# Kernel optimization log

Hardware: AMD Instinct MI355X
Metric: run time of the kernel (lower is better)

## Reference

```python
import jax, jax.numpy as jnp
import numpy as np

N_TOKENS = 65536
HIDDEN = 1024
N_EXPERTS = 64
EPS = 1e-12  # matches F.normalize default eps
NEG_BIG = float(jnp.finfo(jnp.bfloat16).max)  # -torch.finfo(bfloat16).max sentinel


def setup_inputs() -> dict:
    key = jax.random.key(0)
    k1, k2 = jax.random.split(key)
    x = jax.random.normal(k1, (N_TOKENS, HIDDEN), dtype=jnp.float32)
    sim_matrix = jax.random.normal(k2, (HIDDEN, N_EXPERTS), dtype=jnp.float32)  # nn.Parameter(randn)
    gates = jnp.zeros((N_EXPERTS,), dtype=jnp.float32)  # nn.Parameter(zeros)
    return {"x": x, "sim_matrix": sim_matrix, "gates": gates}


def _l2norm(v, axis):
    n = jnp.sqrt(jnp.sum(v * v, axis=axis, keepdims=True))
    return v / jnp.maximum(n, EPS)


def reference(x, sim_matrix, gates):
    # cosine-similarity logits: [N, E]
    logits = jnp.matmul(_l2norm(x, -1), _l2norm(sim_matrix, 0))
    thr = jax.nn.sigmoid(gates)                      # [E]
    pre_activation_logits = logits - thr             # [N, E]
    gated = jax.nn.relu(pre_activation_logits)
    # STE: forward hard 0/1, backward identity
    hard = (gated > 0).astype(x.dtype)
    activation_mask = gated + jax.lax.stop_gradient(hard - gated)
    # topk fallback for rows with zero active experts (vectorized scatter)
    inactive = jnp.sum(hard, axis=1) == 0            # [N]
    k_fallback = N_EXPERTS // 2
    _, topk_idx = jax.lax.top_k(logits, k_fallback)  # [N, k]
    rows = jnp.arange(x.shape[0])
    fb = jnp.zeros_like(logits).at[rows[:, None], topk_idx].set(1.0)
    activation_mask = jnp.where(inactive[:, None], fb, activation_mask)
    # masked softmax over active experts
    masked = jnp.where(activation_mask > 0, gated, -NEG_BIG)
    active_expert_probs = jax.nn.softmax(masked, axis=-1)
    return active_expert_probs, pre_activation_logits, activation_mask
```

## Files before the change

kernel.cpp:

```cpp
#include <hip/hip_runtime.h>
#include <math.h>

#define N_TOK   65536
#define HID     1024
#define NEXP    64
#define EPSF    1e-12f
#define EPSW    4e-5f

typedef __attribute__((ext_vector_type(8))) short s16x8;
typedef __attribute__((ext_vector_type(4))) float f32x4;

__device__ __forceinline__ unsigned short f2bf(float f) {
    unsigned u = __float_as_uint(f);
    unsigned r = u + 0x7fffu + ((u >> 16) & 1u);
    return (unsigned short)(r >> 16);
}
__device__ __forceinline__ float bf2f(unsigned short h) {
    return __uint_as_float(((unsigned)h) << 16);
}
__device__ __forceinline__ unsigned enc_key(float f) {
    unsigned u = __float_as_uint(f);
    return (u & 0x80000000u) ? ~u : (u | 0x80000000u);
}
__device__ __forceinline__ float dec_key(unsigned k) {
    unsigned u = (k & 0x80000000u) ? (k ^ 0x80000000u) : ~k;
    return __uint_as_float(u);
}

__global__ __launch_bounds__(256) void prep_kernel(const float* __restrict__ sim,
                                                   const float* __restrict__ gates,
                                                   float* __restrict__ ws) {
    __shared__ float partial[4][64];
    int e = threadIdx.x & 63;
    int q = threadIdx.x >> 6;
    float s = 0.f;
    for (int h = q * 256; h < q * 256 + 256; ++h) {
        float v = sim[h * NEXP + e];
        s += v * v;
    }
    partial[q][e] = s;
    __syncthreads();
    if (threadIdx.x < 64) {
        float ss = partial[0][e] + partial[1][e] + partial[2][e] + partial[3][e];
        ws[e] = 1.0f / fmaxf(sqrtf(ss), EPSF);
        ws[64 + e] = 1.0f / (1.0f + expf(-gates[e]));
    }
}

__global__ __launch_bounds__(256) void prep2n_kernel(const float* __restrict__ sim,
                                                     const float* __restrict__ ws_ro,
                                                     float* __restrict__ wn) {
    int idx = blockIdx.x * 256 + threadIdx.x;
    wn[idx] = sim[idx] * ws_ro[idx & 63];
}

__global__ __launch_bounds__(256) void prep3_kernel(const float* __restrict__ wn,
                                                    unsigned short* __restrict__ wbh,
                                                    unsigned short* __restrict__ wbl) {
    int i = blockIdx.x * 256 + threadIdx.x;
    int j    = i & 7;
    int lane = (i >> 3) & 63;
    int nt   = (i >> 9) & 3;
    int kt   = i >> 11;
    int k = kt * 32 + ((lane >> 4) & 3) * 8 + j;
    int e = nt * 16 + (lane & 15);
    float v = wn[k * NEXP + e];
    unsigned short h = f2bf(v);
    unsigned short l = f2bf(v - bf2f(h));
    wbh[i] = h; wbl[i] = l;
}

__global__ __launch_bounds__(256) void gate_v12_kernel(const float* __restrict__ x,
                                                       const float* __restrict__ wn,
                                                       const unsigned short* __restrict__ wbh,
                                                       const unsigned short* __restrict__ wbl,
                                                       const float* __restrict__ prep,
                                                       float* __restrict__ out) {
    __shared__ __align__(16) float lg[64][68];
    __shared__ __align__(16) float xrow[HID];
    __shared__ float ss_l[64];
    __shared__ float thr_l[64];
    __shared__ int   flags_i[64];
    __shared__ float part[256];

    const int tid   = threadIdx.x;
    const int lane  = tid & 63;
    const int wv    = tid >> 6;
    const int tbase = blockIdx.x * 64;

    const int arow = lane & 15;
    const int aoct = lane >> 4;
    const float* xg = x + (size_t)(tbase + wv * 16 + arow) * HID + aoct * 8;

    if (tid < 64) thr_l[tid] = prep[64 + tid];

    f32x4 acc[4];
#pragma unroll
    for (int nt = 0; nt < 4; ++nt) acc[nt] = (f32x4){0.f, 0.f, 0.f, 0.f};
    float ss = 0.f;

    const s16x8* bh_g = (const s16x8*)wbh;
    const s16x8* bl_g = (const s16x8*)wbl;

    float4 xv0 = *(const float4*)(xg);
    float4 xv1 = *(const float4*)(xg + 4);

#pragma unroll 2
    for (int c = 0; c < 32; ++c) {
        float4 nx0, nx1;
        if (c < 31) {
            nx0 = *(const float4*)(xg + (c + 1) * 32);
            nx1 = *(const float4*)(xg + (c + 1) * 32 + 4);
        }
        s16x8 bh[4], bl[4];
#pragma unroll
        for (int nt = 0; nt < 4; ++nt) {
            bh[nt] = bh_g[(c * 4 + nt) * 64 + lane];
            bl[nt] = bl_g[(c * 4 + nt) * 64 + lane];
        }
        const float a[8] = { xv0.x, xv0.y, xv0.z, xv0.w, xv1.x, xv1.y, xv1.z, xv1.w };
        s16x8 ah, al;
#pragma unroll
        for (int i = 0; i < 8; ++i) {
            ss = fmaf(a[i], a[i], ss);
            unsigned short h = f2bf(a[i]);
            ah[i] = (short)h;
            al[i] = (short)f2bf(a[i] - bf2f(h));
        }
#pragma unroll
        for (int nt = 0; nt < 4; ++nt)
            acc[nt] = __builtin_amdgcn_mfma_f32_16x16x32_bf16(al, bh[nt], acc[nt], 0, 0, 0);
#pragma unroll
        for (int nt = 0; nt < 4; ++nt)
            acc[nt] = __builtin_amdgcn_mfma_f32_16x16x32_bf16(ah, bl[nt], acc[nt], 0, 0, 0);
#pragma unroll
        for (int nt = 0; nt < 4; ++nt)
            acc[nt] = __builtin_amdgcn_mfma_f32_16x16x32_bf16(ah, bh[nt], acc[nt], 0, 0, 0);
        xv0 = nx0; xv1 = nx1;
    }

    ss += __shfl_xor(ss, 16);
    ss += __shfl_xor(ss, 32);
    if (lane < 16) ss_l[wv * 16 + lane] = ss;

#pragma unroll
    for (int nt = 0; nt < 4; ++nt)
#pragma unroll
        for (int r = 0; r < 4; ++r)
            lg[wv * 16 + aoct * 4 + r][nt * 16 + arow] = acc[nt][r];
    __syncthreads();

    const int tg = lane >> 3;
    const int eg = lane & 7;
    const int e0 = eg * 8;
    const size_t out_pre  = (size_t)N_TOK * NEXP;
    const size_t out_mask = 2 * (size_t)N_TOK * NEXP;

#pragma unroll
    for (int j = 0; j < 2; ++j) {
        const int tl = wv * 16 + tg * 2 + j;
        const int t  = tbase + tl;
        const float inv = 1.0f / fmaxf(sqrtf(ss_l[tl]), EPSF);

        float logit[8], pre[8];
        int active[8];
        int myact = 0;
#pragma unroll
        for (int i = 0; i < 8; ++i) {
            logit[i] = lg[tl][e0 + i] * inv;
            pre[i]   = logit[i] - thr_l[e0 + i];
            active[i] = pre[i] > 0.f;
            myact += active[i];
        }
        *(float4*)&out[out_pre + (size_t)t * NEXP + e0]     = make_float4(pre[0], pre[1], pre[2], pre[3]);
        *(float4*)&out[out_pre + (size_t)t * NEXP + e0 + 4] = make_float4(pre[4], pre[5], pre[6], pre[7]);

        int rowact = myact;
        rowact += __shfl_xor(rowact, 1, 8);
        rowact += __shfl_xor(rowact, 2, 8);
        rowact += __shfl_xor(rowact, 4, 8);

        int flag;
        if (rowact > 0) {
            float mn = 1e30f;
#pragma unroll
            for (int i = 0; i < 8; ++i) mn = fminf(mn, fabsf(pre[i]));
            mn = fminf(mn, __shfl_xor(mn, 1, 8));
            mn = fminf(mn, __shfl_xor(mn, 2, 8));
            mn = fminf(mn, __shfl_xor(mn, 4, 8));
            flag = (mn <= EPSW);
            if (!flag) {
                float gated[8], probs[8], mask[8];
#pragma unroll
                for (int i = 0; i < 8; ++i) gated[i] = fmaxf(pre[i], 0.f);
                float m = -INFINITY;
#pragma unroll
                for (int i = 0; i < 8; ++i) m = fmaxf(m, active[i] ? gated[i] : -INFINITY);
                m = fmaxf(m, __shfl_xor(m, 1, 8));
                m = fmaxf(m, __shfl_xor(m, 2, 8));
                m = fmaxf(m, __shfl_xor(m, 4, 8));
                float s = 0.f;
#pragma unroll
                for (int i = 0; i < 8; ++i) {
                    float ev = active[i] ? expf(gated[i] - m) : 0.f;
                    probs[i] = ev; s += ev;
                }
                s += __shfl_xor(s, 1, 8);
                s += __shfl_xor(s, 2, 8);
                s += __shfl_xor(s, 4, 8);
                float rs = 1.0f / s;
#pragma unroll
                for (int i = 0; i < 8; ++i) { probs[i] *= rs; mask[i] = active[i] ? 1.f : 0.f; }
                size_t row = (size_t)t * NEXP + e0;
                *(float4*)&out[row]                = make_float4(probs[0], probs[1], probs[2], probs[3]);
                *(float4*)&out[row + 4]            = make_float4(probs[4], probs[5], probs[6], probs[7]);
                *(float4*)&out[out_mask + row]     = make_float4(mask[0], mask[1], mask[2], mask[3]);
                *(float4*)&out[out_mask + row + 4] = make_float4(mask[4], mask[5], mask[6], mask[7]);
            }
        } else {
            unsigned key[8];
#pragma unroll
            for (int i = 0; i < 8; ++i) key[i] = enc_key(logit[i]);
            unsigned cand = 0u;
            for (int bit = 31; bit >= 0; --bit) {
                unsigned test = cand | (1u << bit);
                int c = 0;
#pragma unroll
                for (int i = 0; i < 8; ++i) c += (key[i] >= test);
                c += __shfl_xor(c, 1, 8);
                c += __shfl_xor(c, 2, 8);
                c += __shfl_xor(c, 4, 8);
                if (c >= 32) cand = test;
            }
            const float val32 = dec_key(cand);
            int nhi = 0, nlo = 0, nam = 0;
#pragma unroll
            for (int i = 0; i < 8; ++i) {
                nhi += logit[i] > val32 + EPSW;
                nlo += logit[i] > val32 - EPSW;
                nam += pre[i] > -EPSW;
            }
            nhi += __shfl_xor(nhi, 1, 8); nhi += __shfl_xor(nhi, 2, 8); nhi += __shfl_xor(nhi, 4, 8);
            nlo += __shfl_xor(nlo, 1, 8); nlo += __shfl_xor(nlo, 2, 8); nlo += __shfl_xor(nlo, 4, 8);
            nam += __shfl_xor(nam, 1, 8); nam += __shfl_xor(nam, 2, 8); nam += __shfl_xor(nam, 4, 8);
            flag = !(nhi == 31 && nlo == 32) || (nam > 0);
            if (!flag) {
                float probs[8], mask[8];
#pragma unroll
                for (int i = 0; i < 8; ++i) {
                    int sel = logit[i] > val32 - EPSW;
                    mask[i]  = sel ? 1.f : 0.f;
                    probs[i] = sel ? 0.03125f : 0.f;
                }
                size_t row = (size_t)t * NEXP + e0;
                *(float4*)&out[row]                = make_float4(probs[0], probs[1], probs[2], probs[3]);
                *(float4*)&out[row + 4]            = make_float4(probs[4], probs[5], probs[6], probs[7]);
                *(float4*)&out[out_mask + row]     = make_float4(mask[0], mask[1], mask[2], mask[3]);
                *(float4*)&out[out_mask + row + 4] = make_float4(mask[4], mask[5], mask[6], mask[7]);
            }
        }
        if (eg == 0) flags_i[tl] = flag;
    }
    __syncthreads();

    for (int tf = 0; tf < 64; ++tf) {
        if (flags_i[tf] == 0) continue;
        {
            float4 v = *(const float4*)&x[(size_t)(tbase + tf) * HID + tid * 4];
            *(float4*)&xrow[tid * 4] = v;
        }
        __syncthreads();
        const int e = tid & 63;
        const int q = tid >> 6;
        const float* wp = wn + (size_t)q * 256 * NEXP + e;
        const float* xr = xrow + q * 256;
        float dot = 0.f;
#pragma unroll 8
        for (int k2 = 0; k2 < 256; ++k2)
            dot = fmaf(xr[k2], wp[(size_t)k2 * NEXP], dot);
        part[q * 64 + e] = dot;
        __syncthreads();
        if (tid < 64) {
            const float inv = 1.0f / fmaxf(sqrtf(ss_l[tf]), EPSF);
            const float lgv = ((part[e] + part[64 + e]) + (part[128 + e] + part[192 + e])) * inv;
            const float pr = lgv - thr_l[e];
            unsigned long long act = __ballot(pr > 0.f);
            float probs, mask;
            if (act) {
                float g = fmaxf(pr, 0.f);
                float mv = (pr > 0.f) ? g : -INFINITY;
#pragma unroll
                for (int d = 1; d < 64; d <<= 1) mv = fmaxf(mv, __shfl_xor(mv, d));
                float ex = (pr > 0.f) ? expf(g - mv) : 0.f;
                float s = ex;
#pragma unroll
                for (int d = 1; d < 64; d <<= 1) s += __shfl_xor(s, d);
                probs = ex / s;
                mask  = (pr > 0.f) ? 1.f : 0.f;
            } else {
                unsigned key = enc_key(lgv);
                unsigned cand = 0u;
                for (int bit = 31; bit >= 0; --bit) {
                    unsigned test = cand | (1u << bit);
                    int c = __popcll(__ballot(key >= test));
                    if (c >= 32) cand = test;
                }
                int need = 32 - __popcll(__ballot(key > cand));
                unsigned long long em = __ballot(key == cand);
                unsigned long long mlt = e ? (~0ull >> (64 - e)) : 0ull;
                int below = __popcll(em & mlt);
                int sel = (key > cand) || ((key == cand) && (below < need));
                probs = sel ? 0.03125f : 0.f;
                mask  = sel ? 1.f : 0.f;
            }
            size_t row = (size_t)(tbase + tf) * NEXP;
            out[row + e] = probs;
            out[out_mask + row + e] = mask;
        }
        __syncthreads();
    }
}

__global__ __launch_bounds__(256) void gate_v10_kernel(const float* __restrict__ x,
                                                       const float* __restrict__ wn,
                                                       const float* __restrict__ prep,
                                                       float* __restrict__ out) {
    __shared__ __align__(16) float smem[8704];
    float* ss_part = smem + 8448;
    const int tid  = threadIdx.x;
    const int lane = tid & 63;
    const int wv   = tid >> 6;
    const int tg   = lane >> 3;
    const int eg   = lane & 7;
    const int e0   = eg * 8;
    const int tbase = blockIdx.x * 64;
    const int kbase = wv * 256;
    float* xsw = smem + wv * 2112;
    const float4* xq4 = (const float4*)(x + (size_t)(tbase + lane) * HID + kbase);
    float acc[8][8];
#pragma unroll
    for (int t = 0; t < 8; ++t)
#pragma unroll
        for (int e = 0; e < 8; ++e) acc[t][e] = 0.f;
    float ss = 0.f;
    {
        float4 f0 = xq4[0], f1 = xq4[1];
        const float4* wq4 = (const float4*)(wn + (size_t)kbase * NEXP) + lane * 2;
        float4 w0 = wq4[0], w1 = wq4[1];
        const float a[8] = { f0.x, f0.y, f0.z, f0.w, f1.x, f1.y, f1.z, f1.w };
#pragma unroll
        for (int i = 0; i < 8; ++i) { ss = fmaf(a[i], a[i], ss); xsw[i * 68 + lane] = a[i]; }
        *(float4*)&xsw[1088 + lane * 8]     = w0;
        *(float4*)&xsw[1088 + lane * 8 + 4] = w1;
    }
#define FMA8x8(XA, XB, WA, WB)                                              \
    do {                                                                    \
        const float xv_[8] = { XA.x, XA.y, XA.z, XA.w, XB.x, XB.y, XB.z, XB.w }; \
        const float wv_[8] = { WA.x, WA.y, WA.z, WA.w, WB.x, WB.y, WB.z, WB.w }; \
        _Pragma("unroll")                                                   \
        for (int t_ = 0; t_ < 8; ++t_)                                      \
            _Pragma("unroll")                                               \
            for (int e_ = 0; e_ < 8; ++e_)                                  \
                acc[t_][e_] = fmaf(xv_[t_], wv_[e_], acc[t_][e_]);          \
    } while (0)
#pragma unroll 1
    for (int c = 0; c < 32; ++c) {
        float4 sx0, sx1, sw0, sw1;
        if (c < 31) {
            sx0 = xq4[(c + 1) * 2];
            sx1 = xq4[(c + 1) * 2 + 1];
            const float4* wq4 = (const float4*)(wn + (size_t)(kbase + (c + 1) * 8) * NEXP) + lane * 2;
            sw0 = wq4[0]; sw1 = wq4[1];
        }
        const float* xb = xsw + (c & 1) * 544;
        const float* wb = xsw + 1088 + (c & 1) * 512;
#pragma unroll
        for (int k = 0; k < 8; ++k) {
            const float4 xa = *(const float4*)&xb[k * 68 + tg * 8];
            const float4 xc = *(const float4*)&xb[k * 68 + tg * 8 + 4];
            const float4 wa = *(const float4*)&wb[k * 64 + e0];
            const float4 wc = *(const float4*)&wb[k * 64 + e0 + 4];
            FMA8x8(xa, xc, wa, wc);
        }
        if (c < 31) {
            float* xn = xsw + ((c + 1) & 1) * 544;
            float* wl = xsw + 1088 + ((c + 1) & 1) * 512;
            const float a[8] = { sx0.x, sx0.y, sx0.z, sx0.w, sx1.x, sx1.y, sx1.z, sx1.w };
#pragma unroll
            for (int i = 0; i < 8; ++i) { ss = fmaf(a[i], a[i], ss); xn[i * 68 + lane] = a[i]; }
            *(float4*)&wl[lane * 8]     = sw0;
            *(float4*)&wl[lane * 8 + 4] = sw1;
        }
    }
#undef FMA8x8
    ss_part[wv * 64 + lane] = ss;
    __syncthreads();
    if (wv < 2) {
        float* reg = smem + wv * 4224;
#pragma unroll
        for (int j = 0; j < 8; ++j) {
            float* p = &reg[(tg * 8 + j) * 65 + e0];
            *(float4*)(p)     = make_float4(acc[j][0], acc[j][1], acc[j][2], acc[j][3]);
            *(float4*)(p + 4) = make_float4(acc[j][4], acc[j][5], acc[j][6], acc[j][7]);
        }
    }
    __syncthreads();
    if (wv >= 2) {
        float* reg = smem + (wv - 2) * 4224;
#pragma unroll
        for (int j = 0; j < 8; ++j) {
            float* p = &reg[(tg * 8 + j) * 65 + e0];
            float4 p0 = *(const float4*)(p);
            float4 p1 = *(const float4*)(p + 4);
            p0.x += acc[j][0]; p0.y += acc[j][1]; p0.z += acc[j][2]; p0.w += acc[j][3];
            p1.x += acc[j][4]; p1.y += acc[j][5]; p1.z += acc[j][6]; p1.w += acc[j][7];
            *(float4*)(p) = p0; *(float4*)(p + 4) = p1;
        }
    }
    __syncthreads();
    float thr[8];
#pragma unroll
    for (int i = 0; i < 8; ++i) thr[i] = prep[64 + e0 + i];
    const size_t out_pre  = (size_t)N_TOK * NEXP;
    const size_t out_mask = 2 * (size_t)N_TOK * NEXP;
    const float* regA = smem;
    const float* regB = smem + 4224;
#pragma unroll
    for (int j = 0; j < 2; ++j) {
        const int tl = wv * 16 + tg * 2 + j;
        const int t  = tbase + tl;
        const float sst = (ss_part[tl] + ss_part[64 + tl]) + (ss_part[128 + tl] + ss_part[192 + tl]);
        const float inv = 1.0f / fmaxf(sqrtf(sst), EPSF);
        float4 aA0 = *(const float4*)&regA[tl * 65 + e0];
        float4 aA1 = *(const float4*)&regA[tl * 65 + e0 + 4];
        float4 aB0 = *(const float4*)&regB[tl * 65 + e0];
        float4 aB1 = *(const float4*)&regB[tl * 65 + e0 + 4];
        float logit[8] = { (aA0.x + aB0.x) * inv, (aA0.y + aB0.y) * inv,
                           (aA0.z + aB0.z) * inv, (aA0.w + aB0.w) * inv,
                           (aA1.x + aB1.x) * inv, (aA1.y + aB1.y) * inv,
                           (aA1.z + aB1.z) * inv, (aA1.w + aB1.w) * inv };
        float pre[8], gated[8];
        int active[8];
        int myact = 0;
#pragma unroll
        for (int i = 0; i < 8; ++i) {
            pre[i]   = logit[i] - thr[i];
            gated[i] = fmaxf(pre[i], 0.f);
            active[i] = pre[i] > 0.f;
            myact += active[i];
        }
        int rowact = myact;
        rowact += __shfl_xor(rowact, 1, 8);
        rowact += __shfl_xor(rowact, 2, 8);
        rowact += __shfl_xor(rowact, 4, 8);
        float probs[8], mask[8];
        if (rowact > 0) {
            float m = -INFINITY;
#pragma unroll
            for (int i = 0; i < 8; ++i) m = fmaxf(m, active[i] ? gated[i] : -INFINITY);
            m = fmaxf(m, __shfl_xor(m, 1, 8));
            m = fmaxf(m, __shfl_xor(m, 2, 8));
            m = fmaxf(m, __shfl_xor(m, 4, 8));
            float s = 0.f;
#pragma unroll
            for (int i = 0; i < 8; ++i) { float ev = active[i] ? expf(gated[i] - m) : 0.f; probs[i] = ev; s += ev; }
            s += __shfl_xor(s, 1, 8);
            s += __shfl_xor(s, 2, 8);
            s += __shfl_xor(s, 4, 8);
            float rs = 1.0f / s;
#pragma unroll
            for (int i = 0; i < 8; ++i) { probs[i] *= rs; mask[i] = active[i] ? 1.f : 0.f; }
        } else {
            unsigned key[8];
#pragma unroll
            for (int i = 0; i < 8; ++i) key[i] = enc_key(logit[i]);
            unsigned cand = 0u;
            for (int bit = 31; bit >= 0; --bit) {
                unsigned test = cand | (1u << bit);
                int c = 0;
#pragma unroll
                for (int i = 0; i < 8; ++i) c += (key[i] >= test);
                c += __shfl_xor(c, 1, 8);
                c += __shfl_xor(c, 2, 8);
                c += __shfl_xor(c, 4, 8);
                if (c >= 32) cand = test;
            }
            int cgt = 0;
#pragma unroll
            for (int i = 0; i < 8; ++i) cgt += (key[i] > cand);
            cgt += __shfl_xor(cgt, 1, 8);
            cgt += __shfl_xor(cgt, 2, 8);
            cgt += __shfl_xor(cgt, 4, 8);
            int need_eq = 32 - cgt;
            int eqc = 0;
#pragma unroll
            for (int i = 0; i < 8; ++i) eqc += (key[i] == cand);
            int scan = eqc, tmp;
            tmp = __shfl_up(scan, 1, 8); if (eg >= 1) scan += tmp;
            tmp = __shfl_up(scan, 2, 8); if (eg >= 2) scan += tmp;
            tmp = __shfl_up(scan, 4, 8); if (eg >= 4) scan += tmp;
            int run = scan - eqc;
#pragma unroll
            for (int i = 0; i < 8; ++i) {
                int sel = (key[i] > cand) || ((key[i] == cand) && (run < need_eq));
                run += (key[i] == cand);
                mask[i]  = sel ? 1.f : 0.f;
                probs[i] = sel ? 0.03125f : 0.f;
            }
        }
        const size_t row = (size_t)t * NEXP + e0;
        *(float4*)&out[row]                = make_float4(probs[0], probs[1], probs[2], probs[3]);
        *(float4*)&out[row + 4]            = make_float4(probs[4], probs[5], probs[6], probs[7]);
        *(float4*)&out[out_pre + row]      = make_float4(pre[0], pre[1], pre[2], pre[3]);
        *(float4*)&out[out_pre + row + 4]  = make_float4(pre[4], pre[5], pre[6], pre[7]);
        *(float4*)&out[out_mask + row]     = make_float4(mask[0], mask[1], mask[2], mask[3]);
        *(float4*)&out[out_mask + row + 4] = make_float4(mask[4], mask[5], mask[6], mask[7]);
    }
}

extern "C" void kernel_launch(void* const* d_in, const int* in_sizes, int n_in,
                              void* d_out, int out_size, void* d_ws, size_t ws_size,
                              hipStream_t stream) {
    (void)in_sizes; (void)n_in; (void)out_size;
    const float* x     = (const float*)d_in[0];
    const float* sim   = (const float*)d_in[1];
    const float* gates = (const float*)d_in[2];
    float* out = (float*)d_out;
    float* ws  = (float*)d_ws;

    hipLaunchKernelGGL(prep_kernel, dim3(1), dim3(256), 0, stream, sim, gates, ws);

    const size_t need_v10 = 512 + (size_t)HID * NEXP * sizeof(float);
    const size_t need_v12 = need_v10 + 2 * (size_t)HID * NEXP * sizeof(short);
    if (ws_size >= need_v12) {
        float* wn = ws + 128;
        unsigned short* wbh = (unsigned short*)((char*)ws + 512 + (size_t)HID * NEXP * 4);
        unsigned short* wbl = wbh + (size_t)HID * NEXP;
        hipLaunchKernelGGL(prep2n_kernel, dim3(HID * NEXP / 256), dim3(256), 0, stream,
                           sim, ws, wn);
        hipLaunchKernelGGL(prep3_kernel, dim3(HID * NEXP / 256), dim3(256), 0, stream,
                           wn, wbh, wbl);
        hipLaunchKernelGGL(gate_v12_kernel, dim3(N_TOK / 64), dim3(256), 0, stream,
                           x, wn, wbh, wbl, ws, out);
    } else {
        float* wn = ws + 128;
        hipLaunchKernelGGL(prep2n_kernel, dim3(HID * NEXP / 256), dim3(256), 0, stream,
                           sim, ws, wn);
        hipLaunchKernelGGL(gate_v10_kernel, dim3(N_TOK / 64), dim3(256), 0, stream,
                           x, wn, ws, out);
    }
}
```

Measured before the change: 197.0 us.

## Stage x and weight tiles in double-buffered LDS, split waves by expert tile

The main GEMM loop is restructured. Each wave now owns one 16-expert slice across all 64 tokens, instead of one 16-token slice across all experts. The x rows are converted to bf16 hi/lo once per element and stored in double-buffered shared memory, along with the split weight tiles, and all waves reuse them from there. This removes the redundant global weight loads per wave and overlaps the next chunk's global loads with the current MFMAs. The cost is a __syncthreads on every K step, extra LDS traffic, and a per-row sum of squares that now needs a four-way partial reduction.

```diff
diff --git a/kernel.cpp b/kernel.cpp
--- a/kernel.cpp
+++ b/kernel.cpp
@@ -70,84 +70,129 @@
     wbh[i] = h; wbl[i] = l;
 }
 
-__global__ __launch_bounds__(256) void gate_v12_kernel(const float* __restrict__ x,
+__global__ __launch_bounds__(256) void gate_v14_kernel(const float* __restrict__ x,
                                                        const float* __restrict__ wn,
                                                        const unsigned short* __restrict__ wbh,
                                                        const unsigned short* __restrict__ wbl,
                                                        const float* __restrict__ prep,
                                                        float* __restrict__ out) {
-    __shared__ __align__(16) float lg[64][68];
-    __shared__ __align__(16) float xrow[HID];
-    __shared__ float ss_l[64];
-    __shared__ float thr_l[64];
-    __shared__ int   flags_i[64];
-    __shared__ float part[256];
+    __shared__ __align__(16) float smem[8768];
+    unsigned short* AhU = (unsigned short*)smem;
+    unsigned short* AlU = (unsigned short*)(smem + 2080);
+    unsigned short* BhU = (unsigned short*)(smem + 4352);
+    unsigned short* BlU = (unsigned short*)(smem + 6400);
+    float* xrow    = smem + 4352;
+    float* part    = smem + 5376;
+    int*   flags_i = (int*)(smem + 5632);
+    float* ss_part = smem + 8448;
+    float* thr_l   = smem + 8704;
 
     const int tid   = threadIdx.x;
     const int lane  = tid & 63;
     const int wv    = tid >> 6;
     const int tbase = blockIdx.x * 64;
 
-    const int arow = lane & 15;
-    const int aoct = lane >> 4;
-    const float* xg = x + (size_t)(tbase + wv * 16 + arow) * HID + aoct * 8;
+    const int t_st = tid & 63;
+    const int q_st = tid >> 6;
+    const int fl   = (t_st & 15) + 16 * q_st;
+    const int mt   = t_st >> 4;
+    const float* xrow_g = x + (size_t)(tbase + t_st) * HID;
 
     if (tid < 64) thr_l[tid] = prep[64 + tid];
 
     f32x4 acc[4];
 #pragma unroll
-    for (int nt = 0; nt < 4; ++nt) acc[nt] = (f32x4){0.f, 0.f, 0.f, 0.f};
+    for (int m = 0; m < 4; ++m) acc[m] = (f32x4){0.f, 0.f, 0.f, 0.f};
     float ss = 0.f;
 
     const s16x8* bh_g = (const s16x8*)wbh;
     const s16x8* bl_g = (const s16x8*)wbl;
 
-    float4 xv0 = *(const float4*)(xg);
-    float4 xv1 = *(const float4*)(xg + 4);
-
-#pragma unroll 2
-    for (int c = 0; c < 32; ++c) {
-        float4 nx0, nx1;
-        if (c < 31) {
-            nx0 = *(const float4*)(xg + (c + 1) * 32);
-            nx1 = *(const float4*)(xg + (c + 1) * 32 + 4);
-        }
-        s16x8 bh[4], bl[4];
-#pragma unroll
-        for (int nt = 0; nt < 4; ++nt) {
-            bh[nt] = bh_g[(c * 4 + nt) * 64 + lane];
-            bl[nt] = bl_g[(c * 4 + nt) * 64 + lane];
-        }
-        const float a[8] = { xv0.x, xv0.y, xv0.z, xv0.w, xv1.x, xv1.y, xv1.z, xv1.w };
-        s16x8 ah, al;
+    {
+        float4 v0 = *(const float4*)(xrow_g + q_st * 8);
+        float4 v1 = *(const float4*)(xrow_g + q_st * 8 + 4);
+        s16x8 b0h = bh_g[tid];
+        s16x8 b0l = bl_g[tid];
+        const float a[8] = { v0.x, v0.y, v0.z, v0.w, v1.x, v1.y, v1.z, v1.w };
+        s16x8 hv, lv;
 #pragma unroll
         for (int i = 0; i < 8; ++i) {
             ss = fmaf(a[i], a[i], ss);
             unsigned short h = f2bf(a[i]);
-            ah[i] = (short)h;
-            al[i] = (short)f2bf(a[i] - bf2f(h));
-        }
-#pragma unroll
-        for (int nt = 0; nt < 4; ++nt)
-            acc[nt] = __builtin_amdgcn_mfma_f32_16x16x32_bf16(al, bh[nt], acc[nt], 0, 0, 0);
-#pragma unroll
-        for (int nt = 0; nt < 4; ++nt)
-            acc[nt] = __builtin_amdgcn_mfma_f32_16x16x32_bf16(ah, bl[nt], acc[nt], 0, 0, 0);
-#pragma unroll
-        for (int nt = 0; nt < 4; ++nt)
-            acc[nt] = __builtin_amdgcn_mfma_f32_16x16x32_bf16(ah, bh[nt], acc[nt], 0, 0, 0);
-        xv0 = nx0; xv1 = nx1;
-    }
-
-    ss += __shfl_xor(ss, 16);
-    ss += __shfl_xor(ss, 32);
-    if (lane < 16) ss_l[wv * 16 + lane] = ss;
-
-#pragma unroll
-    for (int nt = 0; nt < 4; ++nt)
-#pragma unroll
-        for (int r = 0; r < 4; ++r)
-            lg[wv * 16 + aoct * 4 + r][nt * 16 + arow] = acc[nt][r];
+            hv[i] = (short)h;
+            lv[i] = (short)f2bf(a[i] - bf2f(h));
+        }
+        int slot = mt * 65 + fl;
+        *(s16x8*)&AhU[slot * 8] = hv;
+        *(s16x8*)&AlU[slot * 8] = lv;
+        *(s16x8*)&BhU[tid * 8] = b0h;
+        *(s16x8*)&BlU[tid * 8] = b0l;
+    }
+    __syncthreads();
+
+#pragma unroll 1
+    for (int c = 0; c < 32; ++c) {
+        const int buf = c & 1;
+        float4 nv0, nv1;
+        s16x8 nBh, nBl;
+        if (c < 31) {
+            nv0 = *(const float4*)(xrow_g + (c + 1) * 32 + q_st * 8);
+            nv1 = *(const float4*)(xrow_g + (c + 1) * 32 + q_st * 8 + 4);
+            nBh = bh_g[(c + 1) * 256 + tid];
+            nBl = bl_g[(c + 1) * 256 + tid];
+        }
+
+        s16x8 ah[4], al[4];
+#pragma unroll
+        for (int m = 0; m < 4; ++m) {
+            int base = ((buf << 2) + m) * 65 * 8 + lane * 8;
+            ah[m] = *(const s16x8*)&AhU[base];
+            al[m] = *(const s16x8*)&AlU[base];
+        }
+        s16x8 bhf = *(const s16x8*)&BhU[(buf * 256 + wv * 64 + lane) * 8];
+        s16x8 blf = *(const s16x8*)&BlU[(buf * 256 + wv * 64 + lane) * 8];
+#pragma unroll
+        for (int m = 0; m < 4; ++m)
+            acc[m] = __builtin_amdgcn_mfma_f32_16x16x32_bf16(al[m], bhf, acc[m], 0, 0, 0);
+#pragma unroll
+        for (int m = 0; m < 4; ++m)
+            acc[m] = __builtin_amdgcn_mfma_f32_16x16x32_bf16(ah[m], blf, acc[m], 0, 0, 0);
+#pragma unroll
+        for (int m = 0; m < 4; ++m)
+            acc[m] = __builtin_amdgcn_mfma_f32_16x16x32_bf16(ah[m], bhf, acc[m], 0, 0, 0);
+
+        if (c < 31) {
+            const float a[8] = { nv0.x, nv0.y, nv0.z, nv0.w, nv1.x, nv1.y, nv1.z, nv1.w };
+            s16x8 hv, lv;
+#pragma unroll
+            for (int i = 0; i < 8; ++i) {
+                ss = fmaf(a[i], a[i], ss);
+                unsigned short h = f2bf(a[i]);
+                hv[i] = (short)h;
+                lv[i] = (short)f2bf(a[i] - bf2f(h));
+            }
+            int slot = (((buf ^ 1) << 2) + mt) * 65 + fl;
+            *(s16x8*)&AhU[slot * 8] = hv;
+            *(s16x8*)&AlU[slot * 8] = lv;
+            *(s16x8*)&BhU[((buf ^ 1) * 256 + tid) * 8] = nBh;
+            *(s16x8*)&BlU[((buf ^ 1) * 256 + tid) * 8] = nBl;
+        }
+        __syncthreads();
+    }
+
+    ss_part[q_st * 64 + t_st] = ss;
+    {
+        float* lg = smem;
+#pragma unroll
+        for (int m = 0; m < 4; ++m) {
+#pragma unroll
+            for (int r = 0; r < 4; ++r) {
+                int tok = m * 16 + (lane >> 4) * 4 + r;
+                int e   = wv * 16 + (lane & 15);
+                lg[tok * 68 + e] = acc[m][r];
+            }
+        }
+    }
     __syncthreads();
 
     const int tg = lane >> 3;
@@ -160,14 +205,16 @@
     for (int j = 0; j < 2; ++j) {
         const int tl = wv * 16 + tg * 2 + j;
         const int t  = tbase + tl;
-        const float inv = 1.0f / fmaxf(sqrtf(ss_l[tl]), EPSF);
+        const float sst = (ss_part[tl] + ss_part[64 + tl])
+                        + (ss_part[128 + tl] + ss_part[192 + tl]);
+        const float inv = 1.0f / fmaxf(sqrtf(sst), EPSF);
 
         float logit[8], pre[8];
         int active[8];
         int myact = 0;
 #pragma unroll
         for (int i = 0; i < 8; ++i) {
-            logit[i] = lg[tl][e0 + i] * inv;
+            logit[i] = smem[tl * 68 + e0 + i] * inv;
             pre[i]   = logit[i] - thr_l[e0 + i];
             active[i] = pre[i] > 0.f;
             myact += active[i];
@@ -281,7 +328,9 @@
         part[q * 64 + e] = dot;
         __syncthreads();
         if (tid < 64) {
-            const float inv = 1.0f / fmaxf(sqrtf(ss_l[tf]), EPSF);
+            const float sst = (ss_part[tf] + ss_part[64 + tf])
+                            + (ss_part[128 + tf] + ss_part[192 + tf]);
+            const float inv = 1.0f / fmaxf(sqrtf(sst), EPSF);
             const float lgv = ((part[e] + part[64 + e]) + (part[128 + e] + part[192 + e])) * inv;
             const float pr = lgv - thr_l[e];
             unsigned long long act = __ballot(pr > 0.f);
@@ -531,8 +580,8 @@
     hipLaunchKernelGGL(prep_kernel, dim3(1), dim3(256), 0, stream, sim, gates, ws);
 
     const size_t need_v10 = 512 + (size_t)HID * NEXP * sizeof(float);
-    const size_t need_v12 = need_v10 + 2 * (size_t)HID * NEXP * sizeof(short);
-    if (ws_size >= need_v12) {
+    const size_t need_v14 = need_v10 + 2 * (size_t)HID * NEXP * sizeof(short);
+    if (ws_size >= need_v14) {
         float* wn = ws + 128;
         unsigned short* wbh = (unsigned short*)((char*)ws + 512 + (size_t)HID * NEXP * 4);
         unsigned short* wbl = wbh + (size_t)HID * NEXP;
@@ -540,7 +589,7 @@
                            sim, ws, wn);
         hipLaunchKernelGGL(prep3_kernel, dim3(HID * NEXP / 256), dim3(256), 0, stream,
                            wn, wbh, wbl);
-        hipLaunchKernelGGL(gate_v12_kernel, dim3(N_TOK / 64), dim3(256), 0, stream,
+        hipLaunchKernelGGL(gate_v14_kernel, dim3(N_TOK / 64), dim3(256), 0, stream,
                            x, wn, wbh, wbl, ws, out);
     } else {
         float* wn = ws + 128;
```

New measurement: 181.3 us. 1.09x faster.
